# Performance work log

Measured on AMD Instinct MI355X. Metric: run time of the kernel, lower is better.

Reference implementation:

```python
import itertools
import jax, jax.numpy as jnp
from jax import lax
import numpy as np

BS = 16          # block_size
PAD = 2          # split_tree padding = n_conv - 1
NCONV = 3
G = 4            # 4x4x4 grid of active coarse blocks
PADDED = BS + 2 * PAD + 2 * NCONV   # 26, tsdf slice / upsample size
SUB = BS // 2 + 2 * PAD             # 12, prev-block / sub-block spatial size
CIN = 32; COUT = 32
EPS = 1e-5
THRESH = 0.0     # gate: softmax(pred)[:, -1] > 0 is always True -> all blocks routed


def _conv(x, w):
    # torch Conv3d(k=3, s=1, p=0, bias=False)
    return lax.conv_general_dilated(x, w, (1, 1, 1), 'VALID',
                                    dimension_numbers=('NCDHW', 'OIDHW', 'NCDHW'))


def _bn_relu(x, g, b):
    # eval-mode BatchNorm3d (running_mean=0, running_var=1) + ReLU
    s = g * (1.0 / jnp.sqrt(1.0 + EPS))
    return jax.nn.relu(x * s[None, :, None, None, None] + b[None, :, None, None, None])


def _pool2(x):
    return lax.reduce_window(x, -jnp.inf, lax.max, (1, 1, 2, 2, 2), (1, 1, 2, 2, 2), 'VALID')


def setup_inputs() -> dict:
    key = jax.random.key(0)
    ks = jax.random.split(key, 12)
    N = G ** 3
    D = (G - 1) * BS + PADDED  # 74
    f = lambda k, s, sc=0.05: jax.random.normal(k, s, jnp.float32) * sc
    return {
        'prev_blocks': jax.random.normal(ks[0], (N, CIN, SUB, SUB, SUB), jnp.float32),
        'tsdf': jax.random.normal(ks[1], (1, 1, D, D, D), jnp.float32),
        'w_up': f(ks[2], (CIN, CIN, 4, 4, 4)),
        'w_c0': f(ks[3], (COUT, CIN + 1, 3, 3, 3)),
        'g_c0': jnp.ones(COUT, jnp.float32), 'b_c0': jnp.zeros(COUT, jnp.float32),
        'w_c1': f(ks[4], (COUT, COUT, 3, 3, 3)),
        'g_c1': jnp.ones(COUT, jnp.float32), 'b_c1': jnp.zeros(COUT, jnp.float32),
        'w_c2': f(ks[5], (COUT, COUT, 3, 3, 3)),
        'g_c2': jnp.ones(COUT, jnp.float32), 'b_c2': jnp.zeros(COUT, jnp.float32),
        'w_p0': f(ks[6], (16, CIN, 3, 3, 3)),
        'g_p0': jnp.ones(16, jnp.float32), 'b_p0': jnp.zeros(16, jnp.float32),
        'w_p1': f(ks[7], (8, 16, 3, 3, 3)),
        'g_p1': jnp.ones(8, jnp.float32), 'b_p1': jnp.zeros(8, jnp.float32),
        'w_lin': f(ks[8], (3, 8), 0.1),
        'b_lin': jnp.zeros(3, jnp.float32),
    }


def reference(prev_blocks, tsdf, w_up, w_c0, g_c0, b_c0, w_c1, g_c1, b_c1,
              w_c2, g_c2, b_c2, w_p0, g_p0, b_p0, w_p1, g_p1, b_p1, w_lin, b_lin):
    N = prev_blocks.shape[0]
    # --- PredictionBlock per coarse block, batched over all 64 blocks ---
    h = _pool2(_bn_relu(_conv(prev_blocks, w_p0), g_p0, b_p0))  # [N,16,5,5,5]
    h = _pool2(_bn_relu(_conv(h, w_p1), g_p1, b_p1))            # [N,8,1,1,1]
    pred = h.reshape(N, -1) @ w_lin.T + b_lin                   # [N,3]
    # gate (with thresh=0.0 every block is selected; computed for fidelity)
    gate = jax.nn.softmax(pred, axis=-1)[:, -1] > THRESH
    del gate
    # --- upsample selected (= all) blocks: ConvTranspose3d(k=4, s=2, p=0) ---
    up = lax.conv_transpose(prev_blocks, w_up, (2, 2, 2), 'VALID',
                            dimension_numbers=('NCDHW', 'IODHW', 'NCDHW'),
                            transpose_kernel=True)              # [N,CIN,26,26,26]
    # --- slice tsdf pyramid at each block's (x,y,z)*BS origin ---
    starts = jnp.asarray(np.array(list(itertools.product(range(G), repeat=3))) * BS,
                         jnp.int32)                              # [N,3]
    vol = tsdf[0, 0]
    slc = jax.vmap(lambda s: lax.dynamic_slice(vol, (s[0], s[1], s[2]),
                                               (PADDED, PADDED, PADDED)))(starts)
    x = jnp.concatenate([up, slc[:, None]], axis=1)              # [N,CIN+1,26,26,26]
    x = _bn_relu(_conv(x, w_c0), g_c0, b_c0)
    x = _bn_relu(_conv(x, w_c1), g_c1, b_c1)
    x = _bn_relu(_conv(x, w_c2), g_c2, b_c2)                     # [N,COUT,20,20,20]
    # --- split_tree: 8 overlapping children of size SUB per block ---
    n = (x.shape[-1] - 2 * PAD) // 2  # 8
    subs = jnp.stack([x[..., a:a + SUB, b:b + SUB, c:c + SUB]
                      for a, b, c in itertools.product((0, n), repeat=3)], axis=1)
    subtree = subs.reshape(-1, COUT, SUB, SUB, SUB)              # [8N,COUT,12,12,12]
    return (subtree, pred)
```

## Files before the change

### kernel.cpp

```cpp
#include <hip/hip_runtime.h>
#include <math.h>

#define NBLK 64
#define SUBTREE_FLOATS (512ull*32ull*1728ull)

typedef __attribute__((ext_vector_type(8))) short bf16x8;
typedef __attribute__((ext_vector_type(4))) float f32x4;

__device__ __forceinline__ unsigned short f2b(float f) {
    unsigned u = __float_as_uint(f);
    u = u + 0x7FFFu + ((u >> 16) & 1u);
    return (unsigned short)(u >> 16);
}
__device__ __forceinline__ float b2f(unsigned short h) {
    return __uint_as_float(((unsigned)h) << 16);
}
__device__ __forceinline__ float relu_bn(float acc, float g, float b) {
    float s = g * rsqrtf(1.0f + 1e-5f);
    float v = acc * s + b;
    return v > 0.f ? v : 0.f;
}
__device__ __forceinline__ int xcd_lin() {
    int bid = blockIdx.x, nwg = gridDim.x;
    if ((nwg & 7) == 0) {
        int per = nwg >> 3;
        return (bid & 7) * per + (bid >> 3);
    }
    return bid;
}

__global__ __launch_bounds__(128, 2)
void pred_p0(const float* __restrict__ prev, const float* __restrict__ w,
             const float* __restrict__ g, const float* __restrict__ b,
             float* __restrict__ h0) {
    int blk = blockIdx.x;
    int n = blk >> 4, co = blk & 15;
    int t = threadIdx.x;
    __shared__ float wlds[864];
    for (int i = t; i < 864; i += 128) wlds[i] = w[co * 864 + i];
    __syncthreads();
    __shared__ float pz5[10 * 10 * 5];
    if (t < 100) {
        int oy = t / 10, ox = t % 10;
        float acc[10];
        #pragma unroll
        for (int i = 0; i < 10; i++) acc[i] = 0.f;
        const float* pb = prev + (size_t)n * 32 * 1728;
        for (int ci = 0; ci < 32; ci++) {
            float wr[27];
            #pragma unroll
            for (int j = 0; j < 27; j++) wr[j] = wlds[ci * 27 + j];
            const float* pc = pb + ci * 1728;
            #pragma unroll
            for (int ky = 0; ky < 3; ky++) {
                #pragma unroll
                for (int kx = 0; kx < 3; kx++) {
                    const float* col = pc + (oy + ky) * 12 + (ox + kx);
                    #pragma unroll
                    for (int j = 0; j < 12; j++) {
                        float u = col[j * 144];
                        #pragma unroll
                        for (int kz = 0; kz < 3; kz++) {
                            int zz = j - kz;
                            if (zz >= 0 && zz < 10)
                                acc[zz] += u * wr[kz * 9 + ky * 3 + kx];
                        }
                    }
                }
            }
        }
        float sc = g[co] * rsqrtf(1.0f + 1e-5f);
        float bi = b[co];
        #pragma unroll
        for (int p = 0; p < 5; p++) {
            float a0 = acc[2 * p]     * sc + bi; a0 = a0 > 0.f ? a0 : 0.f;
            float a1 = acc[2 * p + 1] * sc + bi; a1 = a1 > 0.f ? a1 : 0.f;
            pz5[(oy * 10 + ox) * 5 + p] = fmaxf(a0, a1);
        }
    }
    __syncthreads();
    if (t < 125) {
        int pz = t / 25, py = (t / 5) % 5, px = t % 5;
        float m = -INFINITY;
        #pragma unroll
        for (int dy = 0; dy < 2; dy++)
        #pragma unroll
        for (int dx = 0; dx < 2; dx++)
            m = fmaxf(m, pz5[((2 * py + dy) * 10 + 2 * px + dx) * 5 + pz]);
        h0[(n * 16 + co) * 125 + pz * 25 + py * 5 + px] = m;
    }
}

__global__ void pred_p1(const float* __restrict__ h0, const float* __restrict__ w,
                        const float* __restrict__ g, const float* __restrict__ b,
                        const float* __restrict__ wlin, const float* __restrict__ blin,
                        float* __restrict__ pred_out) {
    int n = blockIdx.x;
    __shared__ float conv[216];
    __shared__ float pooled[8];
    int t = threadIdx.x;
    if (t < 216) {
        int co = t / 27, r = t % 27;
        int oz = r / 9, oy = (r / 3) % 3, ox = r % 3;
        float acc = 0.f;
        for (int ci = 0; ci < 16; ci++) {
            const float* hc = h0 + (n * 16 + ci) * 125 + oz * 25 + oy * 5 + ox;
            const float* wc = w + (co * 16 + ci) * 27;
            #pragma unroll
            for (int kz = 0; kz < 3; kz++)
            #pragma unroll
            for (int ky = 0; ky < 3; ky++)
            #pragma unroll
            for (int kx = 0; kx < 3; kx++)
                acc += hc[kz * 25 + ky * 5 + kx] * wc[kz * 9 + ky * 3 + kx];
        }
        conv[t] = relu_bn(acc, g[co], b[co]);
    }
    __syncthreads();
    if (t < 8) {
        float m = -INFINITY;
        for (int dz = 0; dz < 2; dz++)
        for (int dy = 0; dy < 2; dy++)
        for (int dx = 0; dx < 2; dx++)
            m = fmaxf(m, conv[t * 27 + dz * 9 + dy * 3 + dx]);
        pooled[t] = m;
    }
    __syncthreads();
    if (t < 3) {
        float acc = blin[t];
        #pragma unroll
        for (int j = 0; j < 8; j++) acc += pooled[j] * wlin[t * 8 + j];
        pred_out[n * 3 + t] = acc;
    }
}

__global__ __launch_bounds__(256)
void ptcvt(const float* __restrict__ prev, unsigned short* __restrict__ Pt) {
    int n = blockIdx.x;
    const float* pb = prev + (size_t)n * 32 * 1728;
    unsigned short* ob = Pt + (size_t)n * 2744 * 32;
    for (int pos = threadIdx.x; pos < 2744; pos += 256) {
        int x = pos % 14, y = (pos / 14) % 14, zz = pos / 196;
        ushort4* o = (ushort4*)(ob + (size_t)pos * 32);
        if (x >= 1 && x <= 12 && y >= 1 && y <= 12 && zz >= 1 && zz <= 12) {
            int src = (zz - 1) * 144 + (y - 1) * 12 + (x - 1);
            unsigned short v[32];
            #pragma unroll
            for (int ci = 0; ci < 32; ci++) v[ci] = f2b(pb[(size_t)ci * 1728 + src]);
            #pragma unroll
            for (int j = 0; j < 8; j++)
                o[j] = make_ushort4(v[4 * j], v[4 * j + 1], v[4 * j + 2], v[4 * j + 3]);
        } else {
            #pragma unroll
            for (int j = 0; j < 8; j++) o[j] = make_ushort4(0, 0, 0, 0);
        }
    }
}

__global__ void wupprep(const float* __restrict__ wup, unsigned short* __restrict__ Wt) {
    int i = blockIdx.x * 256 + threadIdx.x;
    int tap = i >> 10, rem = i & 1023, co = rem >> 5, ci = rem & 31;
    Wt[i] = f2b(wup[co * 2048 + ci * 64 + tap]);
}

__global__ __launch_bounds__(256, 2)
void ups_mfma(const unsigned short* __restrict__ Pt,
              const unsigned short* __restrict__ Wt,
              unsigned short* __restrict__ Ut, int n0)
{
    constexpr int TPW = 11;
    int lin = xcd_lin();
    int z  = lin % 26;
    int nl = lin / 26;
    int lane = threadIdx.x & 63, wave = threadIdx.x >> 6;
    int ln = lane & 15, quad = lane >> 4;
    int pz = z & 1, izb = (z >> 1) + 1;
    int py = wave >> 1, px = wave & 1;

    const unsigned short* pbase =
        Pt + (size_t)(n0 + nl) * 2744 * 32 + (size_t)izb * 196 * 32 + quad * 8;

    int nidx[TPW];
    const unsigned short* bptr[TPW];
    #pragma unroll
    for (int t = 0; t < TPW; t++) {
        int n = t * 16 + ln;
        nidx[t] = (n < 169) ? n : 169;
        int nc = (n < 169) ? n : 168;
        int iy = nc / 13 + 1, ix = nc % 13 + 1;
        bptr[t] = pbase + ((size_t)iy * 14 + ix) * 32;
    }
    f32x4 acc[TPW][2];
    #pragma unroll
    for (int t = 0; t < TPW; t++) {
        acc[t][0] = (f32x4){0.f, 0.f, 0.f, 0.f};
        acc[t][1] = (f32x4){0.f, 0.f, 0.f, 0.f};
    }

    #pragma unroll 1
    for (int tap = 0; tap < 8; tap++) {
        int dz = tap >> 2, dy = (tap >> 1) & 1, dx = tap & 1;
        int ptap = (pz + 2 * dz) * 16 + (py + 2 * dy) * 4 + (px + 2 * dx);
        const unsigned short* wp = Wt + ptap * 1024 + ln * 32 + quad * 8;
        bf16x8 Af0 = *(const bf16x8*)wp;
        bf16x8 Af1 = *(const bf16x8*)(wp + 512);
        int off = -((dz * 196 + dy * 14 + dx) * 32);
        #pragma unroll
        for (int t = 0; t < TPW; t++) {
            bf16x8 Bf = *(const bf16x8*)(bptr[t] + off);
            acc[t][0] = __builtin_amdgcn_mfma_f32_16x16x32_bf16(Af0, Bf, acc[t][0], 0, 0, 0);
            acc[t][1] = __builtin_amdgcn_mfma_f32_16x16x32_bf16(Af1, Bf, acc[t][1], 0, 0, 0);
        }
    }

    #pragma unroll
    for (int t = 0; t < TPW; t++) {
        if (nidx[t] >= 169) continue;
        int oy = py + 2 * (nidx[t] / 13);
        int ox = px + 2 * (nidx[t] % 13);
        unsigned short* o = Ut +
            ((size_t)nl * 17576 + (size_t)z * 676 + oy * 26 + ox) * 32 + quad * 4;
        *(ushort4*)o = make_ushort4(f2b(acc[t][0][0]), f2b(acc[t][0][1]),
                                    f2b(acc[t][0][2]), f2b(acc[t][0][3]));
        *(ushort4*)(o + 16) = make_ushort4(f2b(acc[t][1][0]), f2b(acc[t][1][1]),
                                           f2b(acc[t][1][2]), f2b(acc[t][1][3]));
    }
}

__global__ void wprep(const float* __restrict__ w, unsigned short* __restrict__ Wt,
                      int wstride) {
    int i = blockIdx.x * 256 + threadIdx.x;
    if (i >= 27648) return;
    int tap = i >> 10, rem = i & 1023, co = rem >> 5, ci = rem & 31;
    Wt[i] = f2b(w[co * wstride + ci * 27 + tap]);
}

__global__ __launch_bounds__(128)
void vkern(const float* __restrict__ tsdf, const float* __restrict__ w_c0,
           unsigned short* __restrict__ V) {
    int yy = blockIdx.x % 72, zz = blockIdx.x / 72;
    int xx = threadIdx.x;
    if (xx >= 72) return;
    float tv[27];
    #pragma unroll
    for (int kz = 0; kz < 3; kz++)
    #pragma unroll
    for (int ky = 0; ky < 3; ky++)
    #pragma unroll
    for (int kx = 0; kx < 3; kx++)
        tv[kz * 9 + ky * 3 + kx] = tsdf[(size_t)(zz + kz) * 5476 + (yy + ky) * 74 + (xx + kx)];
    unsigned short* o = V + (((size_t)zz * 72 + yy) * 72 + xx) * 32;
    for (int co = 0; co < 32; co++) {
        float a = 0.f;
        const float* wc = w_c0 + co * 891 + 864;
        #pragma unroll
        for (int j = 0; j < 27; j++) a += tv[j] * wc[j];
        o[co] = f2b(a);
    }
}

template<int SIN, int SOUT, int MODE, int TG>
__global__ __launch_bounds__(256, 2)
void conv_mfma(const unsigned short* __restrict__ in_t,
               const unsigned short* __restrict__ Wt,
               const float* __restrict__ gg, const float* __restrict__ bb,
               unsigned short* __restrict__ out_t, float* __restrict__ out_f,
               const unsigned short* __restrict__ V, int n0)
{
    constexpr int NPOS = SOUT * SOUT;
    constexpr int NT = (NPOS + 15) / 16;
    constexpr int ZB = (SOUT + 3) / 4;
    constexpr bool ZEXACT = (SOUT % 4) == 0;
    int lin = xcd_lin();
    int tg = lin % TG;
    int zb = (lin / TG) % ZB;
    int nl = lin / (TG * ZB);
    int z0 = zb * 4;
    int zcnt = ZEXACT ? 4 : ((SOUT - z0) < 4 ? (SOUT - z0) : 4);
    int lane = threadIdx.x & 63, wave = threadIdx.x >> 6;
    int ln = lane & 15, quad = lane >> 4;

    int nidx[2], py[2], px[2];
    const unsigned short* bptr[2];
    const unsigned short* inb = in_t + (size_t)nl * SIN * SIN * SIN * 32;
    #pragma unroll
    for (int t = 0; t < 2; t++) {
        int ti = tg * 8 + wave * 2 + t;
        int n = ti * 16 + ln;
        nidx[t] = (ti < NT && n < NPOS) ? n : NPOS;
        int nc = (nidx[t] < NPOS) ? nidx[t] : (NPOS - 1);
        py[t] = nc / SOUT; px[t] = nc % SOUT;
        bptr[t] = inb + ((size_t)py[t] * SIN + px[t]) * 32 + quad * 8;
    }

    f32x4 acc[4][2][2];
    if constexpr (MODE == 1) {
        int n = n0 + nl;
        int Ab = (n >> 4) * 16, Bb = ((n >> 2) & 3) * 16, Cb = (n & 3) * 16;
        #pragma unroll
        for (int zc = 0; zc < 4; zc++) {
            int zo = z0 + zc;
            #pragma unroll
            for (int t = 0; t < 2; t++) {
                const unsigned short* vp =
                    V + (((size_t)(Ab + zo) * 72 + (Bb + py[t])) * 72 + (Cb + px[t])) * 32
                      + quad * 4;
                ushort4 v0 = *(const ushort4*)vp;
                ushort4 v1 = *(const ushort4*)(vp + 16);
                acc[zc][t][0][0] = b2f(v0.x); acc[zc][t][0][1] = b2f(v0.y);
                acc[zc][t][0][2] = b2f(v0.z); acc[zc][t][0][3] = b2f(v0.w);
                acc[zc][t][1][0] = b2f(v1.x); acc[zc][t][1][1] = b2f(v1.y);
                acc[zc][t][1][2] = b2f(v1.z); acc[zc][t][1][3] = b2f(v1.w);
            }
        }
    } else {
        #pragma unroll
        for (int zc = 0; zc < 4; zc++)
        #pragma unroll
        for (int t = 0; t < 2; t++)
        #pragma unroll
        for (int c = 0; c < 2; c++)
            acc[zc][t][c] = (f32x4){0.f, 0.f, 0.f, 0.f};
    }

    #pragma unroll 1
    for (int kyx = 0; kyx < 9; kyx++) {
        int ky = kyx / 3, kx = kyx % 3;
        const unsigned short* wp = Wt + (size_t)kyx * 1024 + ln * 32 + quad * 8;
        bf16x8 A[3][2];
        #pragma unroll
        for (int kz = 0; kz < 3; kz++) {
            A[kz][0] = *(const bf16x8*)(wp + (size_t)kz * 9216);
            A[kz][1] = *(const bf16x8*)(wp + (size_t)kz * 9216 + 512);
        }
        size_t xyo = ((size_t)ky * SIN + kx) * 32;
        #pragma unroll
        for (int j = 0; j < 6; j++) {
            int zia = z0 + j;
            int zs = zia < SIN ? zia : SIN - 1;
            size_t off = (size_t)zs * SIN * SIN * 32 + xyo;
            bf16x8 B0 = *(const bf16x8*)(bptr[0] + off);
            bf16x8 B1 = *(const bf16x8*)(bptr[1] + off);
            #pragma unroll
            for (int kz = 0; kz < 3; kz++) {
                constexpr int dummy = 0; (void)dummy;
                int zc = j - kz;
                if (zc < 0 || zc >= 4) continue;
                if (ZEXACT || zc < zcnt) {
                    acc[zc][0][0] = __builtin_amdgcn_mfma_f32_16x16x32_bf16(A[kz][0], B0, acc[zc][0][0], 0, 0, 0);
                    acc[zc][0][1] = __builtin_amdgcn_mfma_f32_16x16x32_bf16(A[kz][1], B0, acc[zc][0][1], 0, 0, 0);
                    acc[zc][1][0] = __builtin_amdgcn_mfma_f32_16x16x32_bf16(A[kz][0], B1, acc[zc][1][0], 0, 0, 0);
                    acc[zc][1][1] = __builtin_amdgcn_mfma_f32_16x16x32_bf16(A[kz][1], B1, acc[zc][1][1], 0, 0, 0);
                }
            }
        }
    }

    int cobase = quad * 4;
    f32x4 g0 = *(const f32x4*)(gg + cobase);
    f32x4 g1 = *(const f32x4*)(gg + 16 + cobase);
    f32x4 b0 = *(const f32x4*)(bb + cobase);
    f32x4 b1 = *(const f32x4*)(bb + 16 + cobase);

    #pragma unroll
    for (int zc = 0; zc < 4; zc++) {
        if (!ZEXACT && zc >= zcnt) continue;
        int zo = z0 + zc;
        #pragma unroll
        for (int t = 0; t < 2; t++) {
            if (nidx[t] >= NPOS) continue;
            float v0[4], v1[4];
            #pragma unroll
            for (int r = 0; r < 4; r++) {
                v0[r] = relu_bn(acc[zc][t][0][r], g0[r], b0[r]);
                v1[r] = relu_bn(acc[zc][t][1][r], g1[r], b1[r]);
            }
            if constexpr (MODE != 2) {
                unsigned short* o = out_t +
                    ((size_t)nl * SOUT * SOUT * SOUT + (size_t)zo * NPOS + nidx[t]) * 32 + cobase;
                *(ushort4*)o        = make_ushort4(f2b(v0[0]), f2b(v0[1]), f2b(v0[2]), f2b(v0[3]));
                *(ushort4*)(o + 16) = make_ushort4(f2b(v1[0]), f2b(v1[1]), f2b(v1[2]), f2b(v1[3]));
            } else {
                int n = n0 + nl;
                int oy = py[t], ox = px[t];
                #pragma unroll
                for (int za = 0; za < 2; za++) {
                    int zz = zo - za * 8; if (zz < 0 || zz >= 12) continue;
                    #pragma unroll
                    for (int yb = 0; yb < 2; yb++) {
                        int yy = oy - yb * 8; if (yy < 0 || yy >= 12) continue;
                        #pragma unroll
                        for (int xc = 0; xc < 2; xc++) {
                            int xx = ox - xc * 8; if (xx < 0 || xx >= 12) continue;
                            int s = za * 4 + yb * 2 + xc;
                            float* ob = out_f + ((size_t)n * 8 + s) * 32 * 1728
                                        + zz * 144 + yy * 12 + xx;
                            #pragma unroll
                            for (int r = 0; r < 4; r++) {
                                ob[(size_t)(cobase + r) * 1728]      = v0[r];
                                ob[(size_t)(16 + cobase + r) * 1728] = v1[r];
                            }
                        }
                    }
                }
            }
        }
    }
}

extern "C" void kernel_launch(void* const* d_in, const int* in_sizes, int n_in,
                              void* d_out, int out_size, void* d_ws, size_t ws_size,
                              hipStream_t stream) {
    const float* prev  = (const float*)d_in[0];
    const float* tsdf  = (const float*)d_in[1];
    const float* w_up  = (const float*)d_in[2];
    const float* w_c0  = (const float*)d_in[3];
    const float* g_c0  = (const float*)d_in[4];
    const float* b_c0  = (const float*)d_in[5];
    const float* w_c1  = (const float*)d_in[6];
    const float* g_c1  = (const float*)d_in[7];
    const float* b_c1  = (const float*)d_in[8];
    const float* w_c2  = (const float*)d_in[9];
    const float* g_c2  = (const float*)d_in[10];
    const float* b_c2  = (const float*)d_in[11];
    const float* w_p0  = (const float*)d_in[12];
    const float* g_p0  = (const float*)d_in[13];
    const float* b_p0  = (const float*)d_in[14];
    const float* w_p1  = (const float*)d_in[15];
    const float* g_p1  = (const float*)d_in[16];
    const float* b_p1  = (const float*)d_in[17];
    const float* w_lin = (const float*)d_in[18];
    const float* b_lin = (const float*)d_in[19];

    float* out = (float*)d_out;
    char* wsb  = (char*)d_ws;

    size_t off = 0;
    float* h0 = (float*)(wsb + off);            off += 512000;
    unsigned short* Wt0 = (unsigned short*)(wsb + off); off += 55296;
    unsigned short* Wt1 = (unsigned short*)(wsb + off); off += 55296;
    unsigned short* Wt2 = (unsigned short*)(wsb + off); off += 55296;
    unsigned short* V   = (unsigned short*)(wsb + off); off += 23887872;
    unsigned short* Pt  = (unsigned short*)(wsb + off); off += 11239424;
    unsigned short* WupT= (unsigned short*)(wsb + off); off += 131072;
    size_t fixed = off;

    int chunk = 64;
    while (chunk > 1) {
        size_t need = fixed + (size_t)chunk *
            (1124864ull  + 884736ull  + 681472ull );
        if (need <= ws_size) break;
        chunk >>= 1;
    }
    unsigned short* U_t = (unsigned short*)(wsb + off); off += (size_t)chunk * 1124864;
    unsigned short* X0t = (unsigned short*)(wsb + off); off += (size_t)chunk * 884736;
    unsigned short* X1t = (unsigned short*)(wsb + off);

    pred_p0<<<64 * 16, 128, 0, stream>>>(prev, w_p0, g_p0, b_p0, h0);
    pred_p1<<<64, 256, 0, stream>>>(h0, w_p1, g_p1, b_p1, w_lin, b_lin,
                                    out + SUBTREE_FLOATS);
    ptcvt<<<64, 256, 0, stream>>>(prev, Pt);
    wupprep<<<256, 256, 0, stream>>>(w_up, WupT);
    wprep<<<108, 256, 0, stream>>>(w_c0, Wt0, 891);
    wprep<<<108, 256, 0, stream>>>(w_c1, Wt1, 864);
    wprep<<<108, 256, 0, stream>>>(w_c2, Wt2, 864);
    vkern<<<72 * 72, 128, 0, stream>>>(tsdf, w_c0, V);

    for (int n0 = 0; n0 < NBLK; n0 += chunk) {
        ups_mfma<<<chunk * 26, 256, 0, stream>>>(Pt, WupT, U_t, n0);
        conv_mfma<26, 24, 1, 5><<<chunk * 30, 256, 0, stream>>>(
            U_t, Wt0, g_c0, b_c0, X0t, nullptr, V, n0);
        conv_mfma<24, 22, 0, 4><<<chunk * 24, 256, 0, stream>>>(
            X0t, Wt1, g_c1, b_c1, X1t, nullptr, nullptr, n0);
        conv_mfma<22, 20, 2, 4><<<chunk * 20, 256, 0, stream>>>(
            X1t, Wt2, g_c2, b_c2, nullptr, out, nullptr, n0);
    }
}
```

Baseline: 650.0 us.

## Move prediction-head conv p0 onto bf16 MFMA using shared transposed input

Replaces the scalar fp32 pred_p0 conv, which used 1024 blocks each recomputing from strided global reads, with an MFMA bf16 kernel. The new kernel reuses the padded channels-last bf16 tensor already built for the upsample path, plus a new weight-prep kernel. Fused BN/ReLU and 2x2x2 max pooling are done with a lane shuffle and LDS. ptcvt now launches earlier so the prediction branch can consume its output. Running the prediction branch in bf16 reduces its precision.

```diff
diff --git a/kernel.cpp b/kernel.cpp
--- a/kernel.cpp
+++ b/kernel.cpp
@@ -29,65 +29,122 @@
     return bid;
 }
 
-__global__ __launch_bounds__(128, 2)
-void pred_p0(const float* __restrict__ prev, const float* __restrict__ w,
-             const float* __restrict__ g, const float* __restrict__ b,
-             float* __restrict__ h0) {
-    int blk = blockIdx.x;
-    int n = blk >> 4, co = blk & 15;
-    int t = threadIdx.x;
-    __shared__ float wlds[864];
-    for (int i = t; i < 864; i += 128) wlds[i] = w[co * 864 + i];
-    __syncthreads();
-    __shared__ float pz5[10 * 10 * 5];
-    if (t < 100) {
-        int oy = t / 10, ox = t % 10;
-        float acc[10];
-        #pragma unroll
-        for (int i = 0; i < 10; i++) acc[i] = 0.f;
-        const float* pb = prev + (size_t)n * 32 * 1728;
-        for (int ci = 0; ci < 32; ci++) {
-            float wr[27];
-            #pragma unroll
-            for (int j = 0; j < 27; j++) wr[j] = wlds[ci * 27 + j];
-            const float* pc = pb + ci * 1728;
-            #pragma unroll
-            for (int ky = 0; ky < 3; ky++) {
-                #pragma unroll
-                for (int kx = 0; kx < 3; kx++) {
-                    const float* col = pc + (oy + ky) * 12 + (ox + kx);
-                    #pragma unroll
-                    for (int j = 0; j < 12; j++) {
-                        float u = col[j * 144];
-                        #pragma unroll
-                        for (int kz = 0; kz < 3; kz++) {
-                            int zz = j - kz;
-                            if (zz >= 0 && zz < 10)
-                                acc[zz] += u * wr[kz * 9 + ky * 3 + kx];
-                        }
-                    }
+__global__ __launch_bounds__(256)
+void ptcvt(const float* __restrict__ prev, unsigned short* __restrict__ Pt) {
+    int n = blockIdx.x;
+    const float* pb = prev + (size_t)n * 32 * 1728;
+    unsigned short* ob = Pt + (size_t)n * 2744 * 32;
+    for (int pos = threadIdx.x; pos < 2744; pos += 256) {
+        int x = pos % 14, y = (pos / 14) % 14, zz = pos / 196;
+        ushort4* o = (ushort4*)(ob + (size_t)pos * 32);
+        if (x >= 1 && x <= 12 && y >= 1 && y <= 12 && zz >= 1 && zz <= 12) {
+            int src = (zz - 1) * 144 + (y - 1) * 12 + (x - 1);
+            unsigned short v[32];
+            #pragma unroll
+            for (int ci = 0; ci < 32; ci++) v[ci] = f2b(pb[(size_t)ci * 1728 + src]);
+            #pragma unroll
+            for (int j = 0; j < 8; j++)
+                o[j] = make_ushort4(v[4 * j], v[4 * j + 1], v[4 * j + 2], v[4 * j + 3]);
+        } else {
+            #pragma unroll
+            for (int j = 0; j < 8; j++) o[j] = make_ushort4(0, 0, 0, 0);
+        }
+    }
+}
+
+__global__ void wp0prep(const float* __restrict__ w, unsigned short* __restrict__ Wt) {
+    int i = blockIdx.x * 256 + threadIdx.x;
+    if (i >= 13824) return;
+    int tap = i >> 9, rem = i & 511, co = rem >> 5, ci = rem & 31;
+    Wt[i] = f2b(w[co * 864 + ci * 27 + tap]);
+}
+
+__global__ __launch_bounds__(256, 2)
+void pred_p0m(const unsigned short* __restrict__ Pt,
+              const unsigned short* __restrict__ Wp,
+              const float* __restrict__ g, const float* __restrict__ b,
+              float* __restrict__ h0) {
+    int lin = xcd_lin();
+    int zb = lin % 3;
+    int n  = lin / 3;
+    int z0 = zb * 4;
+    int zcnt = (zb == 2) ? 2 : 4;
+    int lane = threadIdx.x & 63, wave = threadIdx.x >> 6;
+    int ln = lane & 15, quad = lane >> 4;
+
+    __shared__ float pool[2][16][10][5];
+
+    const unsigned short* inb = Pt + (size_t)n * 2744 * 32;
+    int nidx[2];
+    const unsigned short* bptr[2];
+    #pragma unroll
+    for (int t = 0; t < 2; t++) {
+        int ti = wave * 2 + t;
+        int p = ti * 16 + ln;
+        nidx[t] = (p < 100) ? p : 100;
+        int pc = (p < 100) ? p : 99;
+        int py = pc / 10, px = pc % 10;
+        bptr[t] = inb + ((size_t)(py + 1) * 14 + (px + 1)) * 32 + quad * 8;
+    }
+    f32x4 acc[4][2];
+    #pragma unroll
+    for (int zc = 0; zc < 4; zc++)
+    #pragma unroll
+    for (int t = 0; t < 2; t++)
+        acc[zc][t] = (f32x4){0.f, 0.f, 0.f, 0.f};
+
+    #pragma unroll 1
+    for (int kyx = 0; kyx < 9; kyx++) {
+        bf16x8 A[3];
+        #pragma unroll
+        for (int kz = 0; kz < 3; kz++)
+            A[kz] = *(const bf16x8*)(Wp + (size_t)(kz * 9 + kyx) * 512 + ln * 32 + quad * 8);
+        size_t xyo = ((size_t)(kyx / 3) * 14 + (kyx % 3)) * 32;
+        #pragma unroll
+        for (int j = 0; j < 6; j++) {
+            int zia = z0 + j;
+            int zs = zia < 12 ? zia : 12;
+            size_t off = (size_t)(zs + 1) * 196 * 32 + xyo;
+            bf16x8 B0 = *(const bf16x8*)(bptr[0] + off);
+            bf16x8 B1 = *(const bf16x8*)(bptr[1] + off);
+            #pragma unroll
+            for (int kz = 0; kz < 3; kz++) {
+                int zc = j - kz;
+                if (zc < 0 || zc >= 4) continue;
+                acc[zc][0] = __builtin_amdgcn_mfma_f32_16x16x32_bf16(A[kz], B0, acc[zc][0], 0, 0, 0);
+                acc[zc][1] = __builtin_amdgcn_mfma_f32_16x16x32_bf16(A[kz], B1, acc[zc][1], 0, 0, 0);
+            }
+        }
+    }
+
+    f32x4 gv = *(const f32x4*)(g + quad * 4);
+    f32x4 bv = *(const f32x4*)(b + quad * 4);
+    int zpcnt = zcnt >> 1;
+    #pragma unroll
+    for (int zp = 0; zp < 2; zp++) {
+        if (zp >= zpcnt) continue;
+        #pragma unroll
+        for (int t = 0; t < 2; t++) {
+            #pragma unroll
+            for (int r = 0; r < 4; r++) {
+                float a0 = relu_bn(acc[2 * zp][t][r], gv[r], bv[r]);
+                float a1 = relu_bn(acc[2 * zp + 1][t][r], gv[r], bv[r]);
+                float v = fmaxf(a0, a1);
+                v = fmaxf(v, __shfl_xor(v, 1));
+                if (nidx[t] < 100 && !(ln & 1)) {
+                    int pos = nidx[t];
+                    pool[zp][quad * 4 + r][pos / 10][(pos % 10) >> 1] = v;
                 }
             }
         }
-        float sc = g[co] * rsqrtf(1.0f + 1e-5f);
-        float bi = b[co];
-        #pragma unroll
-        for (int p = 0; p < 5; p++) {
-            float a0 = acc[2 * p]     * sc + bi; a0 = a0 > 0.f ? a0 : 0.f;
-            float a1 = acc[2 * p + 1] * sc + bi; a1 = a1 > 0.f ? a1 : 0.f;
-            pz5[(oy * 10 + ox) * 5 + p] = fmaxf(a0, a1);
-        }
     }
     __syncthreads();
-    if (t < 125) {
-        int pz = t / 25, py = (t / 5) % 5, px = t % 5;
-        float m = -INFINITY;
-        #pragma unroll
-        for (int dy = 0; dy < 2; dy++)
-        #pragma unroll
-        for (int dx = 0; dx < 2; dx++)
-            m = fmaxf(m, pz5[((2 * py + dy) * 10 + 2 * px + dx) * 5 + pz]);
-        h0[(n * 16 + co) * 125 + pz * 25 + py * 5 + px] = m;
+    for (int t = threadIdx.x; t < 400; t += 256) {
+        int co = t / 25, r2 = t % 25, py = r2 / 5, px = r2 % 5;
+        for (int zp = 0; zp < zpcnt; zp++) {
+            float v = fmaxf(pool[zp][co][2 * py][px], pool[zp][co][2 * py + 1][px]);
+            h0[((size_t)n * 16 + co) * 125 + (zb * 2 + zp) * 25 + py * 5 + px] = v;
+        }
     }
 }
 
@@ -131,29 +188,6 @@
         #pragma unroll
         for (int j = 0; j < 8; j++) acc += pooled[j] * wlin[t * 8 + j];
         pred_out[n * 3 + t] = acc;
-    }
-}
-
-__global__ __launch_bounds__(256)
-void ptcvt(const float* __restrict__ prev, unsigned short* __restrict__ Pt) {
-    int n = blockIdx.x;
-    const float* pb = prev + (size_t)n * 32 * 1728;
-    unsigned short* ob = Pt + (size_t)n * 2744 * 32;
-    for (int pos = threadIdx.x; pos < 2744; pos += 256) {
-        int x = pos % 14, y = (pos / 14) % 14, zz = pos / 196;
-        ushort4* o = (ushort4*)(ob + (size_t)pos * 32);
-        if (x >= 1 && x <= 12 && y >= 1 && y <= 12 && zz >= 1 && zz <= 12) {
-            int src = (zz - 1) * 144 + (y - 1) * 12 + (x - 1);
-            unsigned short v[32];
-            #pragma unroll
-            for (int ci = 0; ci < 32; ci++) v[ci] = f2b(pb[(size_t)ci * 1728 + src]);
-            #pragma unroll
-            for (int j = 0; j < 8; j++)
-                o[j] = make_ushort4(v[4 * j], v[4 * j + 1], v[4 * j + 2], v[4 * j + 3]);
-        } else {
-            #pragma unroll
-            for (int j = 0; j < 8; j++) o[j] = make_ushort4(0, 0, 0, 0);
-        }
     }
 }
 
@@ -343,7 +377,6 @@
             bf16x8 B1 = *(const bf16x8*)(bptr[1] + off);
             #pragma unroll
             for (int kz = 0; kz < 3; kz++) {
-                constexpr int dummy = 0; (void)dummy;
                 int zc = j - kz;
                 if (zc < 0 || zc >= 4) continue;
                 if (ZEXACT || zc < zcnt) {
@@ -443,6 +476,7 @@
     unsigned short* V   = (unsigned short*)(wsb + off); off += 23887872;
     unsigned short* Pt  = (unsigned short*)(wsb + off); off += 11239424;
     unsigned short* WupT= (unsigned short*)(wsb + off); off += 131072;
+    unsigned short* Wp0 = (unsigned short*)(wsb + off); off += 27648;
     size_t fixed = off;
 
     int chunk = 64;
@@ -456,10 +490,11 @@
     unsigned short* X0t = (unsigned short*)(wsb + off); off += (size_t)chunk * 884736;
     unsigned short* X1t = (unsigned short*)(wsb + off);
 
-    pred_p0<<<64 * 16, 128, 0, stream>>>(prev, w_p0, g_p0, b_p0, h0);
+    ptcvt<<<64, 256, 0, stream>>>(prev, Pt);
+    wp0prep<<<54, 256, 0, stream>>>(w_p0, Wp0);
+    pred_p0m<<<192, 256, 0, stream>>>(Pt, Wp0, g_p0, b_p0, h0);
     pred_p1<<<64, 256, 0, stream>>>(h0, w_p1, g_p1, b_p1, w_lin, b_lin,
                                     out + SUBTREE_FLOATS);
-    ptcvt<<<64, 256, 0, stream>>>(prev, Pt);
     wupprep<<<256, 256, 0, stream>>>(w_up, WupT);
     wprep<<<108, 256, 0, stream>>>(w_c0, Wt0, 891);
     wprep<<<108, 256, 0, stream>>>(w_c1, Wt1, 864);
```

After: 570.1 us. -12.3%, faster.
